# Performance work log

Hardware: AMD Instinct MI355X
Metric: run time of the kernel (lower is better)

Reference implementation:

```python
import jax, jax.numpy as jnp
import numpy as np

BETA = 0.25

def setup_inputs() -> dict:
    key = jax.random.key(0)
    k1, k2 = jax.random.split(key)
    N, D, K = 262144, 64, 512
    encoding = jax.random.normal(k1, (N, D), dtype=jnp.float32)
    # original inits uniform(-1/K, 1/K); scale a normal similarly is fine, but stay faithful:
    weight = jax.random.uniform(k2, (K, D), dtype=jnp.float32, minval=-1.0 / K, maxval=1.0 / K)
    return {"encoding": encoding, "weight": weight}


def reference(encoding, weight):
    # flat view: encoding already [N, D]
    x = encoding  # [N, D]
    # squared euclidean distances; argmin is invariant to sqrt and to ||x||^2 term
    x2 = jnp.sum(x * x, axis=1, keepdims=True)            # [N, 1]
    w2 = jnp.sum(weight * weight, axis=1)                  # [K]
    d2 = x2 - 2.0 * (x @ weight.T) + w2[None, :]           # [N, K]
    idx = jnp.argmin(d2, axis=1)                           # [N]
    quantized = weight[idx]                                # gather == one_hot @ weight, [N, D]

    commitment_loss = jnp.mean((jax.lax.stop_gradient(quantized) - x) ** 2)
    embedding_loss = jnp.mean((quantized - jax.lax.stop_gradient(x)) ** 2)
    vq_loss = commitment_loss * BETA + embedding_loss

    # straight-through estimator
    quantized_st = x + jax.lax.stop_gradient(quantized - x)
    return (idx[:, None], quantized_st, vq_loss)
```

## Files before the change

kernel.cpp:

```cpp
#include <hip/hip_runtime.h>

#define NROWS 262144
#define DDIM  64
#define KCB   512

#define MARGKEY (3u << 17)

#define WS_CNT   0
#define WS_W2P3  1024
#define WS_WHI   4096
#define WS_WMID  69632
#define WS_LIST  135168

typedef __attribute__((ext_vector_type(8))) short short8;
typedef __attribute__((ext_vector_type(4))) float floatx4;
typedef __attribute__((ext_vector_type(2))) unsigned int uintx2;

#if defined(__has_builtin)
#if __has_builtin(__builtin_amdgcn_permlane16_swap) && \
    __has_builtin(__builtin_amdgcn_permlane32_swap)
#define VQ_PLSWAP 1
#endif
#endif

__device__ __forceinline__ unsigned umin2(unsigned a, unsigned b) { return a < b ? a : b; }
__device__ __forceinline__ unsigned umax2(unsigned a, unsigned b) { return a > b ? a : b; }

__device__ __forceinline__ float np_sumsq64(const float* a) {
    float r[8];
#pragma unroll
    for (int j = 0; j < 8; ++j) r[j] = __fmul_rn(a[j], a[j]);
#pragma unroll
    for (int i = 8; i < 64; i += 8) {
#pragma unroll
        for (int j = 0; j < 8; ++j)
            r[j] = __fadd_rn(r[j], __fmul_rn(a[i + j], a[i + j]));
    }
    return __fadd_rn(__fadd_rn(__fadd_rn(r[0], r[1]), __fadd_rn(r[2], r[3])),
                     __fadd_rn(__fadd_rn(r[4], r[5]), __fadd_rn(r[6], r[7])));
}

__device__ __forceinline__ void split2(float e0, float e1, unsigned& hid, unsigned& mid) {
    unsigned u0 = __float_as_uint(e0), u1 = __float_as_uint(e1);
    float r0 = __fsub_rn(e0, __uint_as_float(u0 & 0xFFFF0000u));
    float r1 = __fsub_rn(e1, __uint_as_float(u1 & 0xFFFF0000u));
    hid = (u0 >> 16) | (u1 & 0xFFFF0000u);
    mid = (__float_as_uint(r0) >> 16) | (__float_as_uint(r1) & 0xFFFF0000u);
}

__device__ __forceinline__ void split4(float4 v, uint2& h, uint2& m) {
    unsigned h0, m0, h1, m1;
    split2(v.x, v.y, h0, m0);
    split2(v.z, v.w, h1, m1);
    h = make_uint2(h0, h1);
    m = make_uint2(m0, m1);
}

__device__ __forceinline__ void merge16(unsigned& m1, unsigned& m2) {
#ifdef VQ_PLSWAP
    uintx2 s1 = __builtin_amdgcn_permlane16_swap(m1, m1, false, false);
    uintx2 s2 = __builtin_amdgcn_permlane16_swap(m2, m2, false, false);
    m2 = umin2(umin2(s2[0], s2[1]), umax2(s1[0], s1[1]));
    m1 = umin2(s1[0], s1[1]);
#else
    unsigned o1 = __shfl_xor((int)m1, 16);
    unsigned o2 = __shfl_xor((int)m2, 16);
    m2 = umin2(umin2(m2, o2), umax2(m1, o1));
    m1 = umin2(m1, o1);
#endif
}

__device__ __forceinline__ void merge32(unsigned& m1, unsigned& m2) {
#ifdef VQ_PLSWAP
    uintx2 s1 = __builtin_amdgcn_permlane32_swap(m1, m1, false, false);
    uintx2 s2 = __builtin_amdgcn_permlane32_swap(m2, m2, false, false);
    m2 = umin2(umin2(s2[0], s2[1]), umax2(s1[0], s1[1]));
    m1 = umin2(s1[0], s1[1]);
#else
    unsigned o1 = __shfl_xor((int)m1, 32);
    unsigned o2 = __shfl_xor((int)m2, 32);
    m2 = umin2(umin2(m2, o2), umax2(m1, o1));
    m1 = umin2(m1, o1);
#endif
}

__global__ void vq_prep(const float* __restrict__ w, float* __restrict__ w2p3,
                        unsigned short* __restrict__ whi,
                        unsigned short* __restrict__ wmid,
                        unsigned* __restrict__ cnt, float* __restrict__ loss) {
    const int k = blockIdx.x * blockDim.x + threadIdx.x;
    if (k == 0) { *cnt = 0u; *loss = 0.0f; }
    float ws[64];
    const float4* wp = (const float4*)(w + (size_t)k * DDIM);
#pragma unroll
    for (int j = 0; j < 16; ++j) {
        float4 v = wp[j];
        ws[4 * j + 0] = v.x; ws[4 * j + 1] = v.y;
        ws[4 * j + 2] = v.z; ws[4 * j + 3] = v.w;
    }
    w2p3[k] = __fadd_rn(np_sumsq64(ws), 3.0f);
#pragma unroll
    for (int j = 0; j < 8; ++j) {
        union { unsigned d[4]; short8 s; } H, M;
#pragma unroll
        for (int t = 0; t < 4; ++t) {
            float v0 = __fmul_rn(-2.0f, ws[8 * j + 2 * t]);
            float v1 = __fmul_rn(-2.0f, ws[8 * j + 2 * t + 1]);
            split2(v0, v1, H.d[t], M.d[t]);
        }
        *(short8*)(whi  + (size_t)k * 64 + 8 * j) = H.s;
        *(short8*)(wmid + (size_t)k * 64 + 8 * j) = M.s;
    }
}

__launch_bounds__(256, 4)
__global__ void vq_gemm(const float* __restrict__ x,
                        const unsigned short* __restrict__ whi,
                        const unsigned short* __restrict__ wmid,
                        const float* __restrict__ w2p3g,
                        uint2* __restrict__ mmg) {
    const int tid = threadIdx.x;
    const int wave = tid >> 6, lane = tid & 63;
    const int n16 = lane & 15, quad = lane >> 4;
    const int half = blockIdx.x & 1;
    const int r0 = (blockIdx.x >> 1) * 256;

    __shared__ float w2p3s[256];
    __shared__ __align__(16) unsigned sbh[2][32 * 36];
    __shared__ __align__(16) unsigned sbm[2][32 * 36];
    __shared__ uint2 mm[4][8][32];

    w2p3s[tid] = w2p3g[half * 256 + tid];

    short8 ah[4][2], am[4][2];
#pragma unroll
    for (int f = 0; f < 4; ++f) {
        const int cw = half * 256 + wave * 64 + f * 16 + n16;
#pragma unroll
        for (int s = 0; s < 2; ++s) {
            ah[f][s] = *(const short8*)(whi + (size_t)cw * 64 + s * 32 + quad * 8);
            am[f][s] = *(const short8*)(wmid + (size_t)cw * 64 + s * 32 + quad * 8);
        }
    }

    const int srow = tid >> 4, sc4 = tid & 15;
    {
        float4 v0 = *(const float4*)(x + (size_t)(r0 + srow) * DDIM + 4 * sc4);
        float4 v1 = *(const float4*)(x + (size_t)(r0 + srow + 16) * DDIM + 4 * sc4);
        uint2 h, m;
        split4(v0, h, m);
        *(uint2*)&sbh[0][srow * 36 + 2 * sc4] = h;
        *(uint2*)&sbm[0][srow * 36 + 2 * sc4] = m;
        split4(v1, h, m);
        *(uint2*)&sbh[0][(srow + 16) * 36 + 2 * sc4] = h;
        *(uint2*)&sbm[0][(srow + 16) * 36 + 2 * sc4] = m;
    }
    __syncthreads();

    const unsigned cwq = (unsigned)(half * 256 + wave * 64 + quad * 4);

    for (int it = 0; it < 8; ++it) {
        const int p = it & 1;
        float4 pre0, pre1;
        if (it < 7) {
            pre0 = *(const float4*)(x + (size_t)(r0 + (it + 1) * 32 + srow) * DDIM + 4 * sc4);
            pre1 = *(const float4*)(x + (size_t)(r0 + (it + 1) * 32 + srow + 16) * DDIM + 4 * sc4);
        }

#pragma unroll
        for (int sub = 0; sub < 2; ++sub) {
            const int rb = (sub * 16 + n16) * 36;
            short8 b_h0 = *(const short8*)&sbh[p][rb + quad * 4];
            short8 b_h1 = *(const short8*)&sbh[p][rb + 16 + quad * 4];
            short8 b_m0 = *(const short8*)&sbm[p][rb + quad * 4];
            short8 b_m1 = *(const short8*)&sbm[p][rb + 16 + quad * 4];

            floatx4 acc[4];
#pragma unroll
            for (int f = 0; f < 4; ++f)
                acc[f] = *(const floatx4*)&w2p3s[wave * 64 + f * 16 + quad * 4];
#pragma unroll
            for (int f = 0; f < 4; ++f) {
                acc[f] = __builtin_amdgcn_mfma_f32_16x16x32_bf16(ah[f][0], b_h0, acc[f], 0, 0, 0);
                acc[f] = __builtin_amdgcn_mfma_f32_16x16x32_bf16(ah[f][0], b_m0, acc[f], 0, 0, 0);
                acc[f] = __builtin_amdgcn_mfma_f32_16x16x32_bf16(am[f][0], b_h0, acc[f], 0, 0, 0);
                acc[f] = __builtin_amdgcn_mfma_f32_16x16x32_bf16(ah[f][1], b_h1, acc[f], 0, 0, 0);
                acc[f] = __builtin_amdgcn_mfma_f32_16x16x32_bf16(ah[f][1], b_m1, acc[f], 0, 0, 0);
                acc[f] = __builtin_amdgcn_mfma_f32_16x16x32_bf16(am[f][1], b_h1, acc[f], 0, 0, 0);
            }

            unsigned p1[4], p2[4];
#pragma unroll
            for (int f = 0; f < 4; ++f) {
                unsigned k0 = (__float_as_uint(acc[f][0]) << 9) + (cwq + (unsigned)(f * 16 + 0));
                unsigned k1 = (__float_as_uint(acc[f][1]) << 9) + (cwq + (unsigned)(f * 16 + 1));
                unsigned k2 = (__float_as_uint(acc[f][2]) << 9) + (cwq + (unsigned)(f * 16 + 2));
                unsigned k3 = (__float_as_uint(acc[f][3]) << 9) + (cwq + (unsigned)(f * 16 + 3));
                unsigned lo01 = umin2(k0, k1), hi01 = umax2(k0, k1);
                unsigned lo23 = umin2(k2, k3), hi23 = umax2(k2, k3);
                p1[f] = umin2(lo01, lo23);
                p2[f] = umin2(umax2(lo01, lo23), umin2(hi01, hi23));
            }
            unsigned q1a = umin2(p1[0], p1[1]);
            unsigned q2a = umin2(umax2(p1[0], p1[1]), umin2(p2[0], p2[1]));
            unsigned q1b = umin2(p1[2], p1[3]);
            unsigned q2b = umin2(umax2(p1[2], p1[3]), umin2(p2[2], p2[3]));
            unsigned m1 = umin2(q1a, q1b);
            unsigned m2 = umin2(umax2(q1a, q1b), umin2(q2a, q2b));

            merge16(m1, m2);
            merge32(m1, m2);
            if (lane < 16) mm[wave][it][sub * 16 + n16] = make_uint2(m1, m2);
        }

        if (it < 7) {
            uint2 h, m;
            split4(pre0, h, m);
            *(uint2*)&sbh[p ^ 1][srow * 36 + 2 * sc4] = h;
            *(uint2*)&sbm[p ^ 1][srow * 36 + 2 * sc4] = m;
            split4(pre1, h, m);
            *(uint2*)&sbh[p ^ 1][(srow + 16) * 36 + 2 * sc4] = h;
            *(uint2*)&sbm[p ^ 1][(srow + 16) * 36 + 2 * sc4] = m;
        }
        __syncthreads();
    }

    unsigned a1 = 0xFFFFFFFFu, a2 = 0xFFFFFFFFu;
#pragma unroll
    for (int wv = 0; wv < 4; ++wv) {
        uint2 v = mm[wv][tid >> 5][tid & 31];
        a2 = umin2(umin2(a2, v.y), umax2(a1, v.x));
        a1 = umin2(a1, v.x);
    }
    mmg[(size_t)half * NROWS + (r0 + tid)] = make_uint2(a1, a2);
}

__launch_bounds__(256)
__global__ void vq_merge(const uint2* __restrict__ mmg,
                         float* __restrict__ out_idx,
                         unsigned* __restrict__ cnt,
                         unsigned* __restrict__ list, int listcap) {
    const int row = blockIdx.x * 256 + threadIdx.x;
    const int lane = threadIdx.x & 63;
    uint2 v0 = mmg[row];
    uint2 v1 = mmg[(size_t)NROWS + row];
    unsigned a1 = umin2(v0.x, v1.x);
    unsigned a2 = umin2(umax2(v0.x, v1.x), umin2(v0.y, v1.y));
    out_idx[row] = (float)(a1 & 511u);
    bool flag = (a2 - a1 < MARGKEY);
    unsigned long long mask = __ballot(flag);
    int nw = __popcll(mask);
    unsigned base = 0;
    if (lane == 0 && nw) base = atomicAdd(cnt, (unsigned)nw);
    base = (unsigned)__shfl((int)base, 0);
    if (flag) {
        unsigned pos = base + (unsigned)__popcll(mask & ((1ull << lane) - 1ull));
        if ((int)pos < listcap) list[pos] = (unsigned)row;
    }
}

__launch_bounds__(512, 4)
__global__ void vq_recheck(const float* __restrict__ x,
                           const float* __restrict__ w,
                           const unsigned* __restrict__ cnt,
                           const unsigned* __restrict__ list, int listcap,
                           float* __restrict__ out_idx) {
    const int tid = threadIdx.x;
    unsigned total = *cnt;
    if (total > (unsigned)listcap) total = (unsigned)listcap;
    const unsigned nb = (total + 15) >> 4;
    if (blockIdx.x >= nb) return;

    float wl[64];
    {
        const float4* wp = (const float4*)(w + (size_t)tid * DDIM);
#pragma unroll
        for (int j = 0; j < 16; ++j) {
            float4 v = wp[j];
            wl[4 * j + 0] = v.x; wl[4 * j + 1] = v.y;
            wl[4 * j + 2] = v.z; wl[4 * j + 3] = v.w;
        }
    }
    const float w2l = np_sumsq64(wl);

    __shared__ float d2tile[16][KCB];
    __shared__ int rowbuf[16];
    __shared__ float x2buf[16];

    for (unsigned batch = blockIdx.x; batch < nb; batch += gridDim.x) {
        if (tid < 16) {
            unsigned li = batch * 16 + (unsigned)tid;
            rowbuf[tid] = (li < total) ? (int)list[li] : -1;
        }
        __syncthreads();

        if (tid < 128) {
            const int rl = tid >> 3, j = tid & 7;
            int row = rowbuf[rl]; if (row < 0) row = 0;
            const float* xr = x + (size_t)row * DDIM;
            float a0 = xr[j];
            float r = __fmul_rn(a0, a0);
#pragma unroll
            for (int i = 1; i < 8; ++i) {
                float ai = xr[8 * i + j];
                r = __fadd_rn(r, __fmul_rn(ai, ai));
            }
            float s1 = __fadd_rn(r,  __shfl_xor(r, 1));
            float s2 = __fadd_rn(s1, __shfl_xor(s1, 2));
            float s4 = __fadd_rn(s2, __shfl_xor(s2, 4));
            if (j == 0) x2buf[rl] = s4;
        }
        __syncthreads();

        for (int g = 0; g < 16; g += 4) {
            int ra = rowbuf[g + 0]; if (ra < 0) ra = 0;
            int rb = rowbuf[g + 1]; if (rb < 0) rb = 0;
            int rc = rowbuf[g + 2]; if (rc < 0) rc = 0;
            int rd = rowbuf[g + 3]; if (rd < 0) rd = 0;
            const float* xr0 = x + (size_t)ra * DDIM;
            const float* xr1 = x + (size_t)rb * DDIM;
            const float* xr2 = x + (size_t)rc * DDIM;
            const float* xr3 = x + (size_t)rd * DDIM;
            float m0 = 0.f, m1 = 0.f, m2 = 0.f, m3 = 0.f;
#pragma unroll
            for (int jb = 0; jb < 16; ++jb) {
                float4 a0 = *(const float4*)(xr0 + 4 * jb);
                float4 a1 = *(const float4*)(xr1 + 4 * jb);
                float4 a2 = *(const float4*)(xr2 + 4 * jb);
                float4 a3 = *(const float4*)(xr3 + 4 * jb);
                m0 = __fmaf_rn(a0.x, wl[4 * jb + 0], m0);
                m0 = __fmaf_rn(a0.y, wl[4 * jb + 1], m0);
                m0 = __fmaf_rn(a0.z, wl[4 * jb + 2], m0);
                m0 = __fmaf_rn(a0.w, wl[4 * jb + 3], m0);
                m1 = __fmaf_rn(a1.x, wl[4 * jb + 0], m1);
                m1 = __fmaf_rn(a1.y, wl[4 * jb + 1], m1);
                m1 = __fmaf_rn(a1.z, wl[4 * jb + 2], m1);
                m1 = __fmaf_rn(a1.w, wl[4 * jb + 3], m1);
                m2 = __fmaf_rn(a2.x, wl[4 * jb + 0], m2);
                m2 = __fmaf_rn(a2.y, wl[4 * jb + 1], m2);
                m2 = __fmaf_rn(a2.z, wl[4 * jb + 2], m2);
                m2 = __fmaf_rn(a2.w, wl[4 * jb + 3], m2);
                m3 = __fmaf_rn(a3.x, wl[4 * jb + 0], m3);
                m3 = __fmaf_rn(a3.y, wl[4 * jb + 1], m3);
                m3 = __fmaf_rn(a3.z, wl[4 * jb + 2], m3);
                m3 = __fmaf_rn(a3.w, wl[4 * jb + 3], m3);
            }
            float X0 = x2buf[g + 0], X1 = x2buf[g + 1];
            float X2 = x2buf[g + 2], X3 = x2buf[g + 3];
            d2tile[g + 0][tid] = __fadd_rn(__fsub_rn(X0, __fmul_rn(2.0f, m0)), w2l);
            d2tile[g + 1][tid] = __fadd_rn(__fsub_rn(X1, __fmul_rn(2.0f, m1)), w2l);
            d2tile[g + 2][tid] = __fadd_rn(__fsub_rn(X2, __fmul_rn(2.0f, m2)), w2l);
            d2tile[g + 3][tid] = __fadd_rn(__fsub_rn(X3, __fmul_rn(2.0f, m3)), w2l);
        }
        __syncthreads();

        {
            const int rl  = tid >> 5;
            const int sub = tid & 31;
            float bv = d2tile[rl][sub];
            int   bi = sub;
#pragma unroll
            for (int i = 1; i < 16; ++i) {
                int cc = sub + 32 * i;
                float v = d2tile[rl][cc];
                if (v < bv) { bv = v; bi = cc; }
            }
#pragma unroll
            for (int s = 1; s < 32; s <<= 1) {
                float ov = __shfl_xor(bv, s);
                int   oi = __shfl_xor(bi, s);
                if (ov < bv || (ov == bv && oi < bi)) { bv = ov; bi = oi; }
            }
            if (sub == 0 && rowbuf[rl] >= 0) out_idx[rowbuf[rl]] = (float)bi;
        }
        __syncthreads();
    }
}

__launch_bounds__(256)
__global__ void vq_epilogue(const float* __restrict__ x,
                            const float* __restrict__ w,
                            const float* __restrict__ out_idx_f,
                            float* __restrict__ out_q,
                            float* __restrict__ out_loss) {
    const int row  = blockIdx.x * blockDim.x + threadIdx.x;
    const int bidx = (int)out_idx_f[row];

    const float4* xp = (const float4*)(x + (size_t)row * DDIM);
    const float4* wq = (const float4*)(w + (size_t)bidx * DDIM);
    float4* qo = (float4*)(out_q + (size_t)row * DDIM);
    float ls = 0.0f;
#pragma unroll
    for (int j = 0; j < 16; ++j) {
        float4 xv = xp[j];
        float4 wv = wq[j];
        float e0 = __fsub_rn(wv.x, xv.x), e1 = __fsub_rn(wv.y, xv.y);
        float e2 = __fsub_rn(wv.z, xv.z), e3 = __fsub_rn(wv.w, xv.w);
        ls = fmaf(e0, e0, ls); ls = fmaf(e1, e1, ls);
        ls = fmaf(e2, e2, ls); ls = fmaf(e3, e3, ls);
        float4 q;
        q.x = __fadd_rn(xv.x, e0); q.y = __fadd_rn(xv.y, e1);
        q.z = __fadd_rn(xv.z, e2); q.w = __fadd_rn(xv.w, e3);
        qo[j] = q;
    }
#pragma unroll
    for (int off = 32; off > 0; off >>= 1) ls += __shfl_down(ls, off);
    __shared__ float red[4];
    const int lane = threadIdx.x & 63;
    const int wid  = threadIdx.x >> 6;
    if (lane == 0) red[wid] = ls;
    __syncthreads();
    if (threadIdx.x == 0) {
        float t = (red[0] + red[1]) + (red[2] + red[3]);
        atomicAdd(out_loss, t * (1.25f / (float)(NROWS * DDIM)));
    }
}

extern "C" void kernel_launch(void* const* d_in, const int* in_sizes, int n_in,
                              void* d_out, int out_size, void* d_ws, size_t ws_size,
                              hipStream_t stream) {
    const float* x = (const float*)d_in[0];
    const float* w = (const float*)d_in[1];

    float* out      = (float*)d_out;
    float* out_idx  = out;
    float* out_q    = out + (size_t)NROWS;
    float* out_loss = out + (size_t)NROWS + (size_t)NROWS * DDIM;

    uint2* mmg = (uint2*)out_q;

    char* ws = (char*)d_ws;
    unsigned* cnt  = (unsigned*)(ws + WS_CNT);
    float* w2p3    = (float*)(ws + WS_W2P3);
    unsigned short* whi  = (unsigned short*)(ws + WS_WHI);
    unsigned short* wmid = (unsigned short*)(ws + WS_WMID);
    unsigned* list = (unsigned*)(ws + WS_LIST);
    long cap = ((long)ws_size - WS_LIST) / 4;
    int listcap = cap > 0 ? (cap > NROWS ? NROWS : (int)cap) : 0;

    vq_prep<<<2, 256, 0, stream>>>(w, w2p3, whi, wmid, cnt, out_loss);
    vq_gemm<<<2048, 256, 0, stream>>>(x, whi, wmid, w2p3, mmg);
    vq_merge<<<NROWS / 256, 256, 0, stream>>>(mmg, out_idx, cnt, list, listcap);
    vq_recheck<<<256, 512, 0, stream>>>(x, w, cnt, list, listcap, out_idx);
    vq_epilogue<<<NROWS / 256, 256, 0, stream>>>(x, w, out_idx, out_q, out_loss);
}
```

Measured before the change: 285.3 us.

## Switch distance GEMM to 32x32x16 MFMA tiles with per-lane top-2

Replaces the 16x16x32 bf16 MFMA tiling with 32x32x16 MFMA. Each wave now computes two 32-codeword by 32-row tiles, and the A/B fragment layout changes to match. Each lane reduces 16 accumulator values to a top-2 in registers, so the permlane16 merge step goes away and only one cross-lane merge at 32 remains. The goal is fewer MFMA issues and less shuffle work in the argmin reduction, at the cost of larger accumulator register pressure and a new fragment-indexing scheme that has to be right.

```diff
diff --git a/kernel.cpp b/kernel.cpp
--- a/kernel.cpp
+++ b/kernel.cpp
@@ -14,11 +14,11 @@
 
 typedef __attribute__((ext_vector_type(8))) short short8;
 typedef __attribute__((ext_vector_type(4))) float floatx4;
+typedef __attribute__((ext_vector_type(16))) float floatx16;
 typedef __attribute__((ext_vector_type(2))) unsigned int uintx2;
 
 #if defined(__has_builtin)
-#if __has_builtin(__builtin_amdgcn_permlane16_swap) && \
-    __has_builtin(__builtin_amdgcn_permlane32_swap)
+#if __has_builtin(__builtin_amdgcn_permlane32_swap)
 #define VQ_PLSWAP 1
 #endif
 #endif
@@ -54,20 +54,6 @@
     split2(v.z, v.w, h1, m1);
     h = make_uint2(h0, h1);
     m = make_uint2(m0, m1);
-}
-
-__device__ __forceinline__ void merge16(unsigned& m1, unsigned& m2) {
-#ifdef VQ_PLSWAP
-    uintx2 s1 = __builtin_amdgcn_permlane16_swap(m1, m1, false, false);
-    uintx2 s2 = __builtin_amdgcn_permlane16_swap(m2, m2, false, false);
-    m2 = umin2(umin2(s2[0], s2[1]), umax2(s1[0], s1[1]));
-    m1 = umin2(s1[0], s1[1]);
-#else
-    unsigned o1 = __shfl_xor((int)m1, 16);
-    unsigned o2 = __shfl_xor((int)m2, 16);
-    m2 = umin2(umin2(m2, o2), umax2(m1, o1));
-    m1 = umin2(m1, o1);
-#endif
 }
 
 __device__ __forceinline__ void merge32(unsigned& m1, unsigned& m2) {
@@ -84,6 +70,25 @@
 #endif
 }
 
+__device__ __forceinline__ void top2_16(const unsigned* k, unsigned& m1, unsigned& m2) {
+    unsigned lo[8], hi[8];
+#pragma unroll
+    for (int i = 0; i < 8; ++i) {
+        lo[i] = umin2(k[2 * i], k[2 * i + 1]);
+        hi[i] = umax2(k[2 * i], k[2 * i + 1]);
+    }
+#pragma unroll
+    for (int s = 4; s >= 1; s >>= 1) {
+#pragma unroll
+        for (int i = 0; i < s; ++i) {
+            unsigned l = umin2(lo[i], lo[i + s]);
+            unsigned h = umin2(umax2(lo[i], lo[i + s]), umin2(hi[i], hi[i + s]));
+            lo[i] = l; hi[i] = h;
+        }
+    }
+    m1 = lo[0]; m2 = hi[0];
+}
+
 __global__ void vq_prep(const float* __restrict__ w, float* __restrict__ w2p3,
                         unsigned short* __restrict__ whi,
                         unsigned short* __restrict__ wmid,
@@ -121,7 +126,8 @@
                         uint2* __restrict__ mmg) {
     const int tid = threadIdx.x;
     const int wave = tid >> 6, lane = tid & 63;
-    const int n16 = lane & 15, quad = lane >> 4;
+    const int row32 = lane & 31;
+    const int khalf = lane >> 5;
     const int half = blockIdx.x & 1;
     const int r0 = (blockIdx.x >> 1) * 256;
 
@@ -132,14 +138,15 @@
 
     w2p3s[tid] = w2p3g[half * 256 + tid];
 
-    short8 ah[4][2], am[4][2];
-#pragma unroll
-    for (int f = 0; f < 4; ++f) {
-        const int cw = half * 256 + wave * 64 + f * 16 + n16;
-#pragma unroll
-        for (int s = 0; s < 2; ++s) {
-            ah[f][s] = *(const short8*)(whi + (size_t)cw * 64 + s * 32 + quad * 8);
-            am[f][s] = *(const short8*)(wmid + (size_t)cw * 64 + s * 32 + quad * 8);
+    short8 ah[2][4], am[2][4];
+#pragma unroll
+    for (int tt = 0; tt < 2; ++tt) {
+        const size_t cw = (size_t)(half * 256 + wave * 64 + tt * 32 + row32);
+#pragma unroll
+        for (int t = 0; t < 4; ++t) {
+            const size_t off = cw * 64 + t * 16 + khalf * 8;
+            ah[tt][t] = *(const short8*)(whi + off);
+            am[tt][t] = *(const short8*)(wmid + off);
         }
     }
 
@@ -157,7 +164,7 @@
     }
     __syncthreads();
 
-    const unsigned cwq = (unsigned)(half * 256 + wave * 64 + quad * 4);
+    const unsigned cwk = (unsigned)(half * 256 + wave * 64 + 4 * khalf);
 
     for (int it = 0; it < 8; ++it) {
         const int p = it & 1;
@@ -167,51 +174,42 @@
             pre1 = *(const float4*)(x + (size_t)(r0 + (it + 1) * 32 + srow + 16) * DDIM + 4 * sc4);
         }
 
-#pragma unroll
-        for (int sub = 0; sub < 2; ++sub) {
-            const int rb = (sub * 16 + n16) * 36;
-            short8 b_h0 = *(const short8*)&sbh[p][rb + quad * 4];
-            short8 b_h1 = *(const short8*)&sbh[p][rb + 16 + quad * 4];
-            short8 b_m0 = *(const short8*)&sbm[p][rb + quad * 4];
-            short8 b_m1 = *(const short8*)&sbm[p][rb + 16 + quad * 4];
-
-            floatx4 acc[4];
-#pragma unroll
-            for (int f = 0; f < 4; ++f)
-                acc[f] = *(const floatx4*)&w2p3s[wave * 64 + f * 16 + quad * 4];
-#pragma unroll
-            for (int f = 0; f < 4; ++f) {
-                acc[f] = __builtin_amdgcn_mfma_f32_16x16x32_bf16(ah[f][0], b_h0, acc[f], 0, 0, 0);
-                acc[f] = __builtin_amdgcn_mfma_f32_16x16x32_bf16(ah[f][0], b_m0, acc[f], 0, 0, 0);
-                acc[f] = __builtin_amdgcn_mfma_f32_16x16x32_bf16(am[f][0], b_h0, acc[f], 0, 0, 0);
-                acc[f] = __builtin_amdgcn_mfma_f32_16x16x32_bf16(ah[f][1], b_h1, acc[f], 0, 0, 0);
-                acc[f] = __builtin_amdgcn_mfma_f32_16x16x32_bf16(ah[f][1], b_m1, acc[f], 0, 0, 0);
-                acc[f] = __builtin_amdgcn_mfma_f32_16x16x32_bf16(am[f][1], b_h1, acc[f], 0, 0, 0);
-            }
-
-            unsigned p1[4], p2[4];
-#pragma unroll
-            for (int f = 0; f < 4; ++f) {
-                unsigned k0 = (__float_as_uint(acc[f][0]) << 9) + (cwq + (unsigned)(f * 16 + 0));
-                unsigned k1 = (__float_as_uint(acc[f][1]) << 9) + (cwq + (unsigned)(f * 16 + 1));
-                unsigned k2 = (__float_as_uint(acc[f][2]) << 9) + (cwq + (unsigned)(f * 16 + 2));
-                unsigned k3 = (__float_as_uint(acc[f][3]) << 9) + (cwq + (unsigned)(f * 16 + 3));
-                unsigned lo01 = umin2(k0, k1), hi01 = umax2(k0, k1);
-                unsigned lo23 = umin2(k2, k3), hi23 = umax2(k2, k3);
-                p1[f] = umin2(lo01, lo23);
-                p2[f] = umin2(umax2(lo01, lo23), umin2(hi01, hi23));
-            }
-            unsigned q1a = umin2(p1[0], p1[1]);
-            unsigned q2a = umin2(umax2(p1[0], p1[1]), umin2(p2[0], p2[1]));
-            unsigned q1b = umin2(p1[2], p1[3]);
-            unsigned q2b = umin2(umax2(p1[2], p1[3]), umin2(p2[2], p2[3]));
-            unsigned m1 = umin2(q1a, q1b);
-            unsigned m2 = umin2(umax2(q1a, q1b), umin2(q2a, q2b));
-
-            merge16(m1, m2);
-            merge32(m1, m2);
-            if (lane < 16) mm[wave][it][sub * 16 + n16] = make_uint2(m1, m2);
-        }
+        short8 bh[4], bm[4];
+#pragma unroll
+        for (int t = 0; t < 4; ++t) {
+            bh[t] = *(const short8*)&sbh[p][row32 * 36 + t * 8 + khalf * 4];
+            bm[t] = *(const short8*)&sbm[p][row32 * 36 + t * 8 + khalf * 4];
+        }
+
+        unsigned r1t[2], r2t[2];
+#pragma unroll
+        for (int tt = 0; tt < 2; ++tt) {
+            floatx16 acc;
+            const int wb = wave * 64 + tt * 32 + 4 * khalf;
+#pragma unroll
+            for (int g = 0; g < 4; ++g) {
+                floatx4 v = *(const floatx4*)&w2p3s[wb + 8 * g];
+                acc[4 * g + 0] = v[0]; acc[4 * g + 1] = v[1];
+                acc[4 * g + 2] = v[2]; acc[4 * g + 3] = v[3];
+            }
+#pragma unroll
+            for (int t = 0; t < 4; ++t) {
+                acc = __builtin_amdgcn_mfma_f32_32x32x16_bf16(ah[tt][t], bh[t], acc, 0, 0, 0);
+                acc = __builtin_amdgcn_mfma_f32_32x32x16_bf16(ah[tt][t], bm[t], acc, 0, 0, 0);
+                acc = __builtin_amdgcn_mfma_f32_32x32x16_bf16(am[tt][t], bh[t], acc, 0, 0, 0);
+            }
+            unsigned keys[16];
+#pragma unroll
+            for (int r = 0; r < 16; ++r) {
+                const unsigned moff = (unsigned)((r & 3) + 8 * (r >> 2) + tt * 32);
+                keys[r] = (__float_as_uint(acc[r]) << 9) + cwk + moff;
+            }
+            top2_16(keys, r1t[tt], r2t[tt]);
+        }
+        unsigned m1 = umin2(r1t[0], r1t[1]);
+        unsigned m2 = umin2(umax2(r1t[0], r1t[1]), umin2(r2t[0], r2t[1]));
+        merge32(m1, m2);
+        if (lane < 32) mm[wave][it][row32] = make_uint2(m1, m2);
 
         if (it < 7) {
             uint2 h, m;
```

Result: faster. 261.2 us (-8.4%).
